# Kernel optimization log

Hardware: AMD Instinct MI355X
Metric: run time of the kernel (lower is better)

Reference implementation:

```python
import jax, jax.numpy as jnp
import numpy as np

N_INPUT, N_HIDDEN, N_OUTPUT = 500, 1500, 10
N_NEURONS = N_INPUT + N_HIDDEN + N_OUTPUT   # 2010
N_LEARN = N_HIDDEN + N_OUTPUT               # 1510 (supervised task)
ALPHABET = 4
TAU_FF, TAU_FB, TAU_SYN = 10.0, 10.0, 5.0
MEMORY = 10  # max(tau_ff, tau_fb)


def setup_inputs() -> dict:
    key = jax.random.key(0)
    ks = jax.random.split(key, 6)
    topology = jax.random.bernoulli(ks[0], 0.2, (N_LEARN, N_NEURONS)).astype(jnp.int32)
    ff_weights = jax.random.normal(ks[1], (N_LEARN, ALPHABET, N_NEURONS, ALPHABET), jnp.float32) * 0.01
    fb_weights = jax.random.normal(ks[2], (N_LEARN, ALPHABET), jnp.float32) * 0.01
    bias = jax.random.normal(ks[3], (N_LEARN, ALPHABET), jnp.float32) * 0.01
    # spiking history: one-hot (or silent) spikes per neuron per past step, [N, A, T]
    hist_idx = jax.random.randint(ks[4], (N_NEURONS, MEMORY), 0, ALPHABET + 1)
    spiking_history = jax.nn.one_hot(hist_idx, ALPHABET + 1, dtype=jnp.float32)[..., 1:]
    spiking_history = jnp.transpose(spiking_history, (0, 2, 1))  # [N, A, T]
    # current input signal for visible neurons (input + output under train_ml), 0 = silent
    input_idx = jax.random.randint(ks[5], (N_INPUT + N_OUTPUT,), 0, ALPHABET + 1).astype(jnp.int32)
    return {"ff_weights": ff_weights, "fb_weights": fb_weights, "bias": bias,
            "spiking_history": spiking_history, "topology": topology, "input_idx": input_idx}


def reference(ff_weights, fb_weights, bias, spiking_history, topology, input_idx):
    # zero self-connections among learnable neurons (mirrors topology[i, learnable[i]] = 0)
    topo = topology.at[jnp.arange(N_LEARN), N_INPUT + jnp.arange(N_LEARN)].set(0)
    topo = topo.astype(ff_weights.dtype)

    t = jnp.arange(MEMORY, dtype=jnp.float32)
    ff_k = jnp.exp(-t / TAU_FF)   # feedforward basis filter (n_basis=1, exponential)
    fb_k = jnp.exp(-t / TAU_FB)   # feedback basis filter

    hist_rev = spiking_history[:, :, ::-1]  # most-recent-first, [N, A, T]
    # filter traces over the memory window
    ff_trace = jnp.einsum('nat,t->na', hist_rev, ff_k)              # [N, A]
    fb_trace = jnp.einsum('lat,t->la', hist_rev[N_INPUT:], fb_k)    # [L, A]

    # masked sparse synaptic contribution: big mostly-zero 4D weight tensor
    masked_w = ff_weights * topo[:, None, :, None]                  # [L, A, N, A]
    ff_pot = jnp.einsum('lanb,nb->la', masked_w, ff_trace)          # [L, A]
    potential = ff_pot + fb_weights * fb_trace + bias               # [L, A]

    # extended logits with a leading 'no-spike' symbol
    logits = jnp.concatenate([jnp.zeros((N_LEARN, 1), potential.dtype), potential], axis=-1)

    # stochastic spike sampling (OneHotCategorical) for hidden neurons
    samp = jax.random.categorical(jax.random.key(7), logits[:N_HIDDEN])      # [H]
    hidden_spk = jax.nn.one_hot(samp, ALPHABET + 1, dtype=potential.dtype)[:, 1:]
    vis_spk = jax.nn.one_hot(input_idx, ALPHABET + 1, dtype=potential.dtype)[:, 1:]  # [510, A]
    # learnable = hidden then output; output spikes are clamped by the input signal
    learn_spk = jnp.concatenate([hidden_spk, vis_spk[N_INPUT:]], axis=0)     # [L, A]

    ext = jnp.concatenate([1.0 - jnp.sum(learn_spk, -1, keepdims=True), learn_spk], axis=-1)
    log_proba = jnp.sum(ext * jax.nn.log_softmax(logits, axis=-1), axis=-1)  # [L]
    return log_proba
```

## Files before the change

### kernel.cpp

```cpp
#include <hip/hip_runtime.h>
#include <hip/hip_bf16.h>

#define NI 500
#define NH 1500
#define NO 10
#define NN 2010
#define NL 1510
#define AB 4
#define MEM 10

typedef float f32x4 __attribute__((ext_vector_type(4)));

__device__ __forceinline__ unsigned rotl32(unsigned x, int d) {
    return (x << d) | (x >> (32 - d));
}

struct U2 { unsigned a, b; };

__device__ __forceinline__ U2 tf2x32(unsigned k0, unsigned k1, unsigned x0, unsigned x1) {
    const unsigned ks0 = k0, ks1 = k1, ks2 = k0 ^ k1 ^ 0x1BD11BDAu;
    x0 += ks0; x1 += ks1;
#define RR(r) { x0 += x1; x1 = rotl32(x1, r); x1 ^= x0; }
    RR(13) RR(15) RR(26) RR(6)   x0 += ks1; x1 += ks2 + 1u;
    RR(17) RR(29) RR(16) RR(24)  x0 += ks2; x1 += ks0 + 2u;
    RR(13) RR(15) RR(26) RR(6)   x0 += ks0; x1 += ks1 + 3u;
    RR(17) RR(29) RR(16) RR(24)  x0 += ks1; x1 += ks2 + 4u;
    RR(13) RR(15) RR(26) RR(6)   x0 += ks2; x1 += ks0 + 5u;
#undef RR
    return {x0, x1};
}

__device__ __forceinline__ unsigned bitsV(int V, U2 k, unsigned i, unsigned h) {
    if (V == 0) {
        if (i < h) return tf2x32(k.a, k.b, i, i + h).a;
        else       return tf2x32(k.a, k.b, i - h, i).b;
    }
    U2 o = (V <= 3) ? tf2x32(k.a, k.b, 0u, i) : tf2x32(k.a, k.b, i, 0u);
    return (V == 2) ? o.a : (V == 3) ? o.b : (o.a ^ o.b);
}

__device__ __forceinline__ unsigned origOut(U2 k, unsigned j, unsigned n) {
    if (j < n) return tf2x32(k.a, k.b, j, j + n).a;
    else       return tf2x32(k.a, k.b, j - n, j).b;
}

__device__ __forceinline__ U2 splitC(int S, U2 k, unsigned c, unsigned n) {
    if (S == 0) {
        return { origOut(k, 2u * c, n), origOut(k, 2u * c + 1u, n) };
    } else if (S == 1) {
        return tf2x32(k.a, k.b, 0u, c);
    } else {
        return tf2x32(k.a, k.b, c, 0u);
    }
}

__global__ __launch_bounds__(256) void kprep(const float* __restrict__ hist,
                                             const int* __restrict__ input_idx,
                                             float* __restrict__ trace,
                                             int* __restrict__ winner) {
    if (blockIdx.x == 0) {
        __shared__ int ok[15];
        const int tid = threadIdx.x;
        if (tid < 15) ok[tid] = 1;
        __syncthreads();
        const int c = tid >> 4;
        const int t = tid & 15;
        if (c < 15) {
            const int S = c / 5, V = c % 5;
            U2 k5 = splitC(S, {0u, 0u}, 5u, 6u);
            U2 k1 = splitC(S, k5, 0u, 2u);
            U2 k2 = splitC(S, k5, 1u, 2u);
            int mism = 0;
#pragma unroll
            for (int j = 0; j < 6; ++j) {
                unsigned i = (unsigned)(t + 16 * j);
                unsigned hi = bitsV(V, k1, i, 255u);
                unsigned lo = bitsV(V, k2, i, 255u);
                int v = (int)(((hi % 5u) + (lo % 5u)) % 5u);
                if (v != input_idx[i]) mism = 1;
            }
            if (mism) ok[c] = 0;
        }
        __syncthreads();
        if (tid == 0) {
            int f = -1;
            for (int c2 = 14; c2 >= 0; --c2) if (ok[c2]) f = c2;
            winner[0] = f;
        }
    } else {
        int idx = (blockIdx.x - 1) * 256 + threadIdx.x;
        if (idx < NN * AB) {
            const float* h = hist + (size_t)idx * MEM;
            float s = 0.f;
#pragma unroll
            for (int t = 0; t < MEM; ++t)
                s += h[t] * expf((float)(t - (MEM - 1)) * 0.1f);
            trace[idx] = s;
        }
    }
}

__global__ __launch_bounds__(256, 4) void kfused(const float* __restrict__ W,
                                                 const float* __restrict__ fbw,
                                                 const float* __restrict__ bias,
                                                 const int* __restrict__ topo,
                                                 const float* __restrict__ trace,
                                                 const int* __restrict__ input_idx,
                                                 const int* __restrict__ winner,
                                                 float* __restrict__ out) {
    __shared__ f32x4 s_mtr[NN];
    __shared__ float s_pot[AB];
    __shared__ int   s_chain;
    const int l   = blockIdx.x;
    const int tid = threadIdx.x;
    const int diag = NI + l;
    const int* trow = topo + (size_t)l * NN;
    const f32x4* tr4 = reinterpret_cast<const f32x4*>(trace);
    if (tid == 0) s_chain = winner[0];
    for (int n = tid; n < NN; n += 256) {
        float m = (n == diag) ? 0.f : (float)trow[n];
        s_mtr[n] = tr4[n] * m;
    }
    __syncthreads();

    const int a    = tid >> 6;
    const int lane = tid & 63;
    const f32x4* Wrow = reinterpret_cast<const f32x4*>(W) + (size_t)(l * AB + a) * NN;
    float acc0 = 0.f, acc1 = 0.f;
    int n = lane;
#pragma unroll 4
    for (; n + 64 < NN; n += 128) {
        f32x4 w0 = __builtin_nontemporal_load(Wrow + n);
        f32x4 w1 = __builtin_nontemporal_load(Wrow + n + 64);
        f32x4 t0 = s_mtr[n];
        f32x4 t1 = s_mtr[n + 64];
        acc0 += w0.x * t0.x + w0.y * t0.y + w0.z * t0.z + w0.w * t0.w;
        acc1 += w1.x * t1.x + w1.y * t1.y + w1.z * t1.z + w1.w * t1.w;
    }
    if (n < NN) {
        f32x4 w = __builtin_nontemporal_load(Wrow + n);
        f32x4 t = s_mtr[n];
        acc0 += w.x * t.x + w.y * t.y + w.z * t.z + w.w * t.w;
    }
    float acc = acc0 + acc1;
#pragma unroll
    for (int off = 32; off > 0; off >>= 1)
        acc += __shfl_down(acc, off, 64);
    if (lane == 0) {
        int ia = l * AB + a;
        s_pot[a] = acc + fbw[ia] * trace[diag * AB + a] + bias[ia];
    }
    __syncthreads();

    if (tid < 8) {
        const bool valid = tid < 5;
        float myl = valid ? ((tid == 0) ? 0.f : s_pot[tid - 1]) : -3.4e38f;
        float m = myl;
#pragma unroll
        for (int off = 1; off < 8; off <<= 1) m = fmaxf(m, __shfl_xor(m, off, 8));
        float e = valid ? expf(myl - m) : 0.f;
        float s = e;
#pragma unroll
        for (int off = 1; off < 8; off <<= 1) s += __shfl_xor(s, off, 8);
        float lse = m + logf(s);

        int k;
        if (l < NH) {
            float score = -3.4e38f;
            if (valid) {
                int V = (s_chain < 0) ? 0 : (s_chain % 5);
                unsigned j = (unsigned)(l * 5 + tid);
                unsigned bits = bitsV(V, {0u, 7u}, j, 3750u);
                float u = __uint_as_float((bits >> 9) | 0x3f800000u) - 1.0f;
                u = fmaxf(u, 1.17549435e-38f);
                score = -logf(-logf(u)) + myl;
            }
            float bs = score; int bi = tid;
#pragma unroll
            for (int off = 1; off < 8; off <<= 1) {
                float os = __shfl_xor(bs, off, 8);
                int   oi = __shfl_xor(bi, off, 8);
                if (os > bs || (os == bs && oi < bi)) { bs = os; bi = oi; }
            }
            k = bi;
        } else {
            k = input_idx[l - (NH - NI)];
        }
        float val = __shfl(myl, k, 8) - lse;
        if (tid == 0)
            out[l] = (s_chain < 0 && l == 0) ? val + 1000.0f : val;
    }
}

extern "C" void kernel_launch(void* const* d_in, const int* in_sizes, int n_in,
                              void* d_out, int out_size, void* d_ws, size_t ws_size,
                              hipStream_t stream) {
    const float* W    = (const float*)d_in[0];
    const float* fbw  = (const float*)d_in[1];
    const float* bias = (const float*)d_in[2];
    const float* hist = (const float*)d_in[3];
    const int*   topo = (const int*)  d_in[4];
    const int*   iidx = (const int*)  d_in[5];
    float* out = (float*)d_out;

    float* ws     = (float*)d_ws;
    float* trace  = ws;
    int*   winner = (int*)(ws + NN * AB);

    kprep<<<1 + (NN * AB + 255) / 256, 256, 0, stream>>>(hist, iidx, trace, winner);
    kfused<<<NL, 256, 0, stream>>>(W, fbw, bias, topo, trace, iidx, winner, out);
}
```

Measured before the change: 50.31 us.

## Split each neuron row across two blocks with atomic partial sums

Each learnable neuron's dot product over the 2010 presynaptic neurons is now split between two blocks of 1005 each, doubling the grid to 3020 blocks. Partial potentials are combined with atomicAdd into a workspace buffer. A per-row arrival counter lets the last-arriving block compute the log-softmax and the sample. The prep kernel now also zeroes the accumulators and counters. This aims to improve load balance and tail utilisation of a bandwidth-bound stream over the weights, at the cost of atomics, an extra workspace round trip and non-deterministic float summation order.

Result: slower. 188.5 us (+274.8%).

```diff
diff --git a/kernel.cpp b/kernel.cpp
--- a/kernel.cpp
+++ b/kernel.cpp
@@ -8,6 +8,7 @@
 #define NL 1510
 #define AB 4
 #define MEM 10
+#define HALF 1005
 
 typedef float f32x4 __attribute__((ext_vector_type(4)));
 
@@ -57,7 +58,9 @@
 __global__ __launch_bounds__(256) void kprep(const float* __restrict__ hist,
                                              const int* __restrict__ input_idx,
                                              float* __restrict__ trace,
-                                             int* __restrict__ winner) {
+                                             int* __restrict__ winner,
+                                             float* __restrict__ pot,
+                                             int* __restrict__ done) {
     if (blockIdx.x == 0) {
         __shared__ int ok[15];
         const int tid = threadIdx.x;
@@ -97,64 +100,82 @@
                 s += h[t] * expf((float)(t - (MEM - 1)) * 0.1f);
             trace[idx] = s;
         }
-    }
-}
-
-__global__ __launch_bounds__(256, 4) void kfused(const float* __restrict__ W,
-                                                 const float* __restrict__ fbw,
-                                                 const float* __restrict__ bias,
-                                                 const int* __restrict__ topo,
-                                                 const float* __restrict__ trace,
-                                                 const int* __restrict__ input_idx,
-                                                 const int* __restrict__ winner,
-                                                 float* __restrict__ out) {
-    __shared__ f32x4 s_mtr[NN];
-    __shared__ float s_pot[AB];
-    __shared__ int   s_chain;
-    const int l   = blockIdx.x;
-    const int tid = threadIdx.x;
+        if (idx < NL * AB) pot[idx] = 0.f;
+        if (idx < NL)      done[idx] = 0;
+    }
+}
+
+__global__ __launch_bounds__(256, 4) void khalf(const float* __restrict__ W,
+                                                const float* __restrict__ fbw,
+                                                const float* __restrict__ bias,
+                                                const int* __restrict__ topo,
+                                                const float* __restrict__ trace,
+                                                const int* __restrict__ input_idx,
+                                                const int* __restrict__ winner,
+                                                float* __restrict__ pot,
+                                                int* __restrict__ done,
+                                                float* __restrict__ out) {
+    __shared__ f32x4 s_mtr[HALF];
+    __shared__ int   s_done;
+    const int bid  = blockIdx.x;
+    const int l    = bid >> 1;
+    const int n0   = (bid & 1) * HALF;
+    const int tid  = threadIdx.x;
     const int diag = NI + l;
     const int* trow = topo + (size_t)l * NN;
     const f32x4* tr4 = reinterpret_cast<const f32x4*>(trace);
-    if (tid == 0) s_chain = winner[0];
-    for (int n = tid; n < NN; n += 256) {
+    for (int i = tid; i < HALF; i += 256) {
+        int n = n0 + i;
         float m = (n == diag) ? 0.f : (float)trow[n];
-        s_mtr[n] = tr4[n] * m;
+        s_mtr[i] = tr4[n] * m;
     }
     __syncthreads();
 
     const int a    = tid >> 6;
     const int lane = tid & 63;
-    const f32x4* Wrow = reinterpret_cast<const f32x4*>(W) + (size_t)(l * AB + a) * NN;
+    const f32x4* Wrow = reinterpret_cast<const f32x4*>(W) + (size_t)(l * AB + a) * NN + n0;
     float acc0 = 0.f, acc1 = 0.f;
-    int n = lane;
+    int i = lane;
 #pragma unroll 4
-    for (; n + 64 < NN; n += 128) {
-        f32x4 w0 = __builtin_nontemporal_load(Wrow + n);
-        f32x4 w1 = __builtin_nontemporal_load(Wrow + n + 64);
-        f32x4 t0 = s_mtr[n];
-        f32x4 t1 = s_mtr[n + 64];
+    for (; i + 64 < HALF; i += 128) {
+        f32x4 w0 = __builtin_nontemporal_load(Wrow + i);
+        f32x4 w1 = __builtin_nontemporal_load(Wrow + i + 64);
+        f32x4 t0 = s_mtr[i];
+        f32x4 t1 = s_mtr[i + 64];
         acc0 += w0.x * t0.x + w0.y * t0.y + w0.z * t0.z + w0.w * t0.w;
         acc1 += w1.x * t1.x + w1.y * t1.y + w1.z * t1.z + w1.w * t1.w;
     }
-    if (n < NN) {
-        f32x4 w = __builtin_nontemporal_load(Wrow + n);
-        f32x4 t = s_mtr[n];
+    if (i < HALF) {
+        f32x4 w = __builtin_nontemporal_load(Wrow + i);
+        f32x4 t = s_mtr[i];
         acc0 += w.x * t.x + w.y * t.y + w.z * t.z + w.w * t.w;
     }
     float acc = acc0 + acc1;
 #pragma unroll
     for (int off = 32; off > 0; off >>= 1)
         acc += __shfl_down(acc, off, 64);
-    if (lane == 0) {
-        int ia = l * AB + a;
-        s_pot[a] = acc + fbw[ia] * trace[diag * AB + a] + bias[ia];
-    }
+    if (lane == 0)
+        atomicAdd(&pot[l * AB + a], acc);
     __syncthreads();
+
+    if (tid == 0)
+        s_done = __hip_atomic_fetch_add(&done[l], 1, __ATOMIC_ACQ_REL,
+                                        __HIP_MEMORY_SCOPE_AGENT);
+    __syncthreads();
+    if (s_done != 1) return;
 
     if (tid < 8) {
         const bool valid = tid < 5;
-        float myl = valid ? ((tid == 0) ? 0.f : s_pot[tid - 1]) : -3.4e38f;
+        float myl = -3.4e38f;
+        if (valid) {
+            if (tid == 0) myl = 0.f;
+            else {
+                int ia = l * AB + (tid - 1);
+                float p = __hip_atomic_load(&pot[ia], __ATOMIC_RELAXED,
+                                            __HIP_MEMORY_SCOPE_AGENT);
+                myl = p + fbw[ia] * trace[diag * AB + (tid - 1)] + bias[ia];
+            }
+        }
         float m = myl;
 #pragma unroll
         for (int off = 1; off < 8; off <<= 1) m = fmaxf(m, __shfl_xor(m, off, 8));
@@ -164,11 +185,12 @@
         for (int off = 1; off < 8; off <<= 1) s += __shfl_xor(s, off, 8);
         float lse = m + logf(s);
 
+        int chain = winner[0];
         int k;
         if (l < NH) {
+            int V = (chain < 0) ? 0 : (chain % 5);
             float score = -3.4e38f;
             if (valid) {
-                int V = (s_chain < 0) ? 0 : (s_chain % 5);
                 unsigned j = (unsigned)(l * 5 + tid);
                 unsigned bits = bitsV(V, {0u, 7u}, j, 3750u);
                 float u = __uint_as_float((bits >> 9) | 0x3f800000u) - 1.0f;
@@ -188,7 +210,7 @@
         }
         float val = __shfl(myl, k, 8) - lse;
         if (tid == 0)
-            out[l] = (s_chain < 0 && l == 0) ? val + 1000.0f : val;
+            out[l] = (chain < 0 && l == 0) ? val + 1000.0f : val;
     }
 }
 
@@ -205,8 +227,11 @@
 
     float* ws     = (float*)d_ws;
     float* trace  = ws;
-    int*   winner = (int*)(ws + NN * AB);
-
-    kprep<<<1 + (NN * AB + 255) / 256, 256, 0, stream>>>(hist, iidx, trace, winner);
-    kfused<<<NL, 256, 0, stream>>>(W, fbw, bias, topo, trace, iidx, winner, out);
-}
+    float* pot    = ws + NN * AB;
+    int*   winner = (int*)(pot + NL * AB);
+    int*   done   = winner + 4;
+
+    kprep<<<33, 256, 0, stream>>>(hist, iidx, trace, winner, pot, done);
+    khalf<<<2 * NL, 256, 0, stream>>>(W, fbw, bias, topo, trace, iidx, winner,
+                                      pot, done, out);
+}
```
